# Optimization experiments

Measured on AMD Instinct MI355X. Metric: run time of the kernel, lower is better.

The kernel has to match this reference:

```python
import jax, jax.numpy as jnp
import numpy as np

B, E, R, HSZ, HEADS, PROP, RTOKS = 16, 400, 624, 512, 4, 2, 40
N = E + R            # nodes per graph = entities + relations
DFF = HSZ * HEADS    # Block FFN width (l1: hsz -> hsz*heads)


def setup_inputs() -> dict:
    key = jax.random.key(0)
    ks = jax.random.split(key, 12)
    ents = jax.random.normal(ks[0], (B, E, HSZ), jnp.float32)
    rels = jax.random.randint(ks[1], (B, R), 0, RTOKS)
    adj = jax.random.randint(ks[2], (B, N, N), 0, 2)
    # self-loops so no softmax row is fully masked
    d = jnp.arange(N)
    adj = adj.at[:, d, d].set(1)
    renc = jax.random.normal(ks[3], (RTOKS, HSZ)) * (2.0 / (RTOKS + HSZ)) ** 0.5

    def lin(k, fi, fo):  # weights stored (in, out): y = x @ W + b
        return jax.random.normal(k, (PROP, fi, fo)) * (1.0 / fi) ** 0.5

    Wq = lin(ks[4], HSZ, HSZ)
    Wk = lin(ks[5], HSZ, HSZ)
    Wv = lin(ks[6], HSZ, HSZ)
    l1_w = lin(ks[7], HSZ, DFF)
    l1_b = jnp.zeros((PROP, DFF))
    l2_w = lin(ks[8], DFF, HSZ)
    l2_b = jnp.zeros((PROP, HSZ))
    ln1_s = jnp.ones((PROP, HSZ)); ln1_b = jnp.zeros((PROP, HSZ))
    ln2_s = jnp.ones((PROP, HSZ)); ln2_b = jnp.zeros((PROP, HSZ))
    prelu_a = jnp.full((PROP, DFF), 0.25)
    return dict(ents=ents, rels=rels, adj=adj, renc=renc, Wq=Wq, Wk=Wk, Wv=Wv,
                l1_w=l1_w, l1_b=l1_b, l2_w=l2_w, l2_b=l2_b,
                ln1_s=ln1_s, ln1_b=ln1_b, ln2_s=ln2_s, ln2_b=ln2_b,
                prelu_a=prelu_a)


def _layer_norm(x, s, b, eps=1e-5):
    mu = jnp.mean(x, -1, keepdims=True)
    var = jnp.mean((x - mu) ** 2, -1, keepdims=True)
    return (x - mu) * jax.lax.rsqrt(var + eps) * s + b


def _mha(q, kv, adj, Wq, Wk, Wv):
    # GraphWriter MultiHeadAttention: split heads by contiguous chunks,
    # scale by sqrt(key_dim)=sqrt(HSZ), mask where adj==0, residual += query.
    dk = HSZ // HEADS
    Q = (q @ Wq).reshape(B, N, HEADS, dk)
    K = (kv @ Wk).reshape(B, N, HEADS, dk)
    V = (kv @ Wv).reshape(B, N, HEADS, dk)
    scores = jnp.einsum('bnhd,bmhd->bhnm', Q, K) / np.sqrt(HSZ).astype(np.float32)
    scores = jnp.where((adj == 0)[:, None, :, :], -jnp.inf, scores)
    attn = jax.nn.softmax(scores, axis=-1)
    out = jnp.einsum('bhnm,bmhd->bnhd', attn, V).reshape(B, N, HSZ)
    return out + q


def _encode(ents, rels, adj, renc, Wq, Wk, Wv, l1_w, l1_b, l2_w, l2_b,
            ln1_s, ln1_b, ln2_s, ln2_b, prelu_a):
    x = jnp.concatenate([ents, renc[rels]], axis=1)  # (B, N, HSZ)
    for j in range(PROP):  # fixed small number of propagation Blocks
        kv = jax.lax.stop_gradient(x)  # dense path wraps kv in torch.tensor(requires_grad=False)
        out = _mha(x, kv, adj, Wq[j], Wk[j], Wv[j])
        t = _layer_norm(out, ln1_s[j], ln1_b[j])
        h = t @ l1_w[j] + l1_b[j]
        h = jnp.maximum(h, 0) + prelu_a[j] * jnp.minimum(h, 0)  # PReLU
        h = h @ l2_w[j] + l2_b[j]  # dropout p=0 (eval)
        x = _layer_norm(h + t, ln2_s[j], ln2_b[j])
    return x


def reference(ents, rels, adj, renc, Wq, Wk, Wv, l1_w, l1_b, l2_w, l2_b,
              ln1_s, ln1_b, ln2_s, ln2_b, prelu_a):
    nodes = _encode(ents, rels, adj, renc, Wq, Wk, Wv, l1_w, l1_b, l2_w, l2_b,
                    ln1_s, ln1_b, ln2_s, ln2_b, prelu_a)
    glob = nodes[:, E]  # node at index ent_lens[i] (first relation node)
    node_mask = jnp.ones((B, N), dtype=bool)  # ent_lens uniform -> all valid
    return glob, nodes, node_mask
```

## Files before the change

### kernel.cpp

```cpp
#include <hip/hip_runtime.h>
#include <hip/hip_bf16.h>

typedef __bf16 bf16;
typedef __attribute__((ext_vector_type(8))) bf16 bf16x8;
typedef __attribute__((ext_vector_type(4))) float f32x4;

constexpr int B_   = 16;
constexpr int E_   = 400;
constexpr int R_   = 624;
constexpr int N_   = 1024;
constexpr int HSZ_ = 512;
constexpr int DFF_ = 2048;
constexpr int M_   = B_ * N_;

__device__ __forceinline__ void glds16(const void* g, void* l) {
    __builtin_amdgcn_global_load_lds((const __attribute__((address_space(1))) void*)g,
                                     (__attribute__((address_space(3))) void*)l,
                                     16, 0, 0);
}

__global__ __launch_bounds__(256) void transpose_all(const float* __restrict__ Wq,
                                                     const float* __restrict__ Wk,
                                                     const float* __restrict__ Wv,
                                                     const float* __restrict__ l1w,
                                                     const float* __restrict__ l2w,
                                                     bf16* __restrict__ WqkvT,
                                                     bf16* __restrict__ L1T,
                                                     bf16* __restrict__ L2T) {
    __shared__ float tile[32][33];
    int id = blockIdx.x;
    const float* in;
    bf16* out;
    int rows, cols, bx, by;
    if (id < 1536) {
        int grp = id >> 8;
        int loc = id & 255;
        bx = loc & 15; by = loc >> 4;
        rows = 512; cols = 512;
        int j = grp / 3, wsel = grp % 3;
        const float* W = (wsel == 0) ? Wq : (wsel == 1) ? Wk : Wv;
        in  = W + j * 262144;
        out = WqkvT + j * 786432 + wsel * 262144;
    } else if (id < 3584) {
        int loc = id - 1536;
        int j = loc >= 1024; loc &= 1023;
        bx = loc & 63; by = loc >> 6;
        rows = 512; cols = 2048;
        in  = l1w + j * 1048576;
        out = L1T + j * 1048576;
    } else {
        int loc = id - 3584;
        int j = loc >= 1024; loc &= 1023;
        bx = loc & 15; by = loc >> 4;
        rows = 2048; cols = 512;
        in  = l2w + j * 1048576;
        out = L2T + j * 1048576;
    }
    int tx = threadIdx.x & 31, ty = threadIdx.x >> 5;
    int c0 = bx * 32, r0 = by * 32;
    #pragma unroll
    for (int i = 0; i < 32; i += 8)
        tile[ty + i][tx] = in[(size_t)(r0 + ty + i) * cols + (c0 + tx)];
    __syncthreads();
    #pragma unroll
    for (int i = 0; i < 32; i += 8)
        out[(size_t)(c0 + ty + i) * rows + (r0 + tx)] = (bf16)tile[tx][ty + i];
}

__global__ __launch_bounds__(256) void pack_adj(const int* __restrict__ adj,
                                                unsigned* __restrict__ adjw) {
    int gid  = blockIdx.x * 4 + (threadIdx.x >> 6);
    int lane = threadIdx.x & 63;
    int w64  = gid & 15;
    int bn   = gid >> 4;
    int v = adj[(size_t)bn * N_ + w64 * 64 + lane];
    unsigned long long mask = __ballot(v != 0);
    if (lane == 0)  adjw[bn * 32 + w64 * 2]     = (unsigned)mask;
    if (lane == 32) adjw[bn * 32 + w64 * 2 + 1] = (unsigned)(mask >> 32);
}

__global__ __launch_bounds__(256) void build_x(const float* __restrict__ ents,
                                               const int* __restrict__ rels,
                                               const float* __restrict__ renc,
                                               bf16* __restrict__ x) {
    int idx  = blockIdx.x * 256 + threadIdx.x;
    int col8 = (idx & 63) * 8;
    int row  = idx >> 6;
    int b = row >> 10, n = row & 1023;
    const float* src;
    if (n < E_) src = ents + ((size_t)(b * E_ + n)) * HSZ_ + col8;
    else {
        int rt = rels[b * R_ + (n - E_)];
        src = renc + (size_t)rt * HSZ_ + col8;
    }
    float4 a = *(const float4*)src;
    float4 c = *(const float4*)(src + 4);
    bf16x8 v;
    v[0] = (bf16)a.x; v[1] = (bf16)a.y; v[2] = (bf16)a.z; v[3] = (bf16)a.w;
    v[4] = (bf16)c.x; v[5] = (bf16)c.y; v[6] = (bf16)c.z; v[7] = (bf16)c.w;
    *(bf16x8*)(x + (size_t)row * HSZ_ + col8) = v;
}

template <int MODE>
__global__ __launch_bounds__(256) void gemm_bt(const bf16* __restrict__ A,
                                               const bf16* __restrict__ Bt,
                                               const float* __restrict__ biasF,
                                               const float* __restrict__ alphaF,
                                               const bf16* __restrict__ extraB,
                                               bf16* __restrict__ outB,
                                               bf16* __restrict__ outB2,
                                               bf16* __restrict__ outB3,
                                               float* __restrict__ outF,
                                               int Nn, int Kk) {
    __shared__ bf16 As[2][128][64];
    __shared__ bf16 Bs[2][128][64];

    int nwg = gridDim.x * gridDim.y;
    int bid = blockIdx.y * gridDim.x + blockIdx.x;
    int q = nwg >> 3;
    int ng = (bid & 7) * q + (bid >> 3);
    int bx = ng % gridDim.x, by = ng / gridDim.x;

    int n0 = bx * 128, m0 = by * 128;
    int t = threadIdx.x;
    int lane = t & 63, r = lane & 15, quad = lane >> 4;
    int w = t >> 6;
    int wm = w >> 1, wn = w & 1;

    int sRow = t >> 3;
    int xr   = sRow & 7;
    int sColL = (t & 7) * 8;
    int sColG = ((t & 7) ^ xr) * 8;
    const bf16* Ag = A  + (size_t)(m0 + sRow) * Kk + sColG;
    const bf16* Bg = Bt + (size_t)(n0 + sRow) * Kk + sColG;

#define G_STAGE(p_, k0_) do {                                          \
        glds16(Ag + (k0_),           &As[p_][sRow     ][sColL]);       \
        glds16(Ag + 32 * Kk + (k0_), &As[p_][sRow + 32][sColL]);       \
        glds16(Ag + 64 * Kk + (k0_), &As[p_][sRow + 64][sColL]);       \
        glds16(Ag + 96 * Kk + (k0_), &As[p_][sRow + 96][sColL]);       \
        glds16(Bg + (k0_),           &Bs[p_][sRow     ][sColL]);       \
        glds16(Bg + 32 * Kk + (k0_), &Bs[p_][sRow + 32][sColL]);       \
        glds16(Bg + 64 * Kk + (k0_), &Bs[p_][sRow + 64][sColL]);       \
        glds16(Bg + 96 * Kk + (k0_), &Bs[p_][sRow + 96][sColL]);       \
    } while (0)

    f32x4 acc[4][4];
    #pragma unroll
    for (int mt = 0; mt < 4; mt++)
        #pragma unroll
        for (int nt = 0; nt < 4; nt++) acc[mt][nt] = (f32x4){0.f, 0.f, 0.f, 0.f};

    int xa = r & 7;

    G_STAGE(0, 0);
    int ntiles = Kk >> 6;
    for (int tt = 0; tt < ntiles; tt++) {
        int p = tt & 1;
        if (tt + 1 < ntiles) {
            G_STAGE(p ^ 1, (tt + 1) * 64);
            asm volatile("s_waitcnt vmcnt(8)" ::: "memory");
        } else {
            asm volatile("s_waitcnt vmcnt(0)" ::: "memory");
        }
        __builtin_amdgcn_s_barrier();
        __builtin_amdgcn_sched_barrier(0);
        #pragma unroll
        for (int kk = 0; kk < 64; kk += 32) {
            int pc = (((kk >> 3) + quad) ^ xa) * 8;
            bf16x8 af[4], bfr[4];
            #pragma unroll
            for (int mt = 0; mt < 4; mt++)
                af[mt] = *(const bf16x8*)&As[p][wm * 64 + mt * 16 + r][pc];
            #pragma unroll
            for (int nt = 0; nt < 4; nt++)
                bfr[nt] = *(const bf16x8*)&Bs[p][wn * 64 + nt * 16 + r][pc];
            #pragma unroll
            for (int mt = 0; mt < 4; mt++)
                #pragma unroll
                for (int nt = 0; nt < 4; nt++)
                    acc[mt][nt] = __builtin_amdgcn_mfma_f32_16x16x32_bf16(af[mt], bfr[nt], acc[mt][nt], 0, 0, 0);
        }
        __builtin_amdgcn_s_barrier();
        __builtin_amdgcn_sched_barrier(0);
    }
#undef G_STAGE

    #pragma unroll
    for (int mt = 0; mt < 4; mt++) {
        #pragma unroll
        for (int nt = 0; nt < 4; nt++) {
            #pragma unroll
            for (int i = 0; i < 4; i++) {
                int rg = m0 + wm * 64 + mt * 16 + quad * 4 + i;
                int cg = n0 + wn * 64 + nt * 16 + r;
                float v = acc[mt][nt][i];
                if (MODE == 0) {
                    outB[(size_t)rg * Nn + cg] = (bf16)v;
                } else if (MODE == 1) {
                    int bb = rg >> 10, n = rg & 1023;
                    outB[(size_t)(bb * HSZ_ + cg) * N_ + n] = (bf16)v;
                } else if (MODE == 2) {
                    v += biasF[cg];
                    float a = alphaF[cg];
                    v = v > 0.f ? v : a * v;
                    outB[(size_t)rg * Nn + cg] = (bf16)v;
                } else if (MODE == 3) {
                    v += biasF[cg] + (float)extraB[(size_t)rg * Nn + cg];
                    outF[(size_t)rg * Nn + cg] = v;
                } else {
                    if (cg < 512) {
                        outB[(size_t)rg * HSZ_ + cg] = (bf16)v;
                    } else if (cg < 1024) {
                        outB2[(size_t)rg * HSZ_ + (cg - 512)] = (bf16)v;
                    } else {
                        int bb = rg >> 10, n = rg & 1023;
                        outB3[(size_t)(bb * HSZ_ + (cg - 1024)) * N_ + n] = (bf16)v;
                    }
                }
            }
        }
    }
}

__global__ __launch_bounds__(256) void attn_fused(const bf16* __restrict__ Q,
                                                  const bf16* __restrict__ K,
                                                  const bf16* __restrict__ Vt,
                                                  const unsigned* __restrict__ adjw,
                                                  const bf16* __restrict__ xb,
                                                  float* __restrict__ tpre) {
    int blk = blockIdx.x;
    int gr = blk & 7;
    int qb = (blk >> 3) & 7;
    int gq = blk >> 6;
    int g = gq * 8 + gr;
    int b = g >> 2, h = g & 3;

    int tid = threadIdx.x;
    int w = tid >> 6, lane = tid & 63;
    int r = lane & 15, quad = lane >> 4;
    int n0 = qb * 128 + w * 32;

    __shared__ bf16 Ks[64][136];
    __shared__ bf16 Vs[128][72];
    __shared__ bf16 plds[4][32][68];

    int kRow = tid >> 4, kCol = (tid & 15) * 8;
    int vRow = tid >> 3, vCol = (tid & 7) * 8;
    const bf16* Kg = K + (size_t)(b * N_) * HSZ_ + h * 128 + (size_t)kRow * HSZ_ + kCol;
    const bf16* Vg = Vt + (size_t)(b * HSZ_ + h * 128 + vRow) * N_ + vCol;
    bf16* KsP = &Ks[kRow][kCol];
    bf16* VsP = &Vs[vRow][vCol];

    uint4 kp0, kp1, kp2, kp3, vp0, vp1, vp2, vp3;

#define ATTN_ISSUE(it_) do {                                                      \
        const bf16* kg_ = Kg + (size_t)(it_) * 64 * HSZ_;                         \
        const bf16* vg_ = Vg + (it_) * 64;                                        \
        kp0 = *(const uint4*)(kg_);                                               \
        kp1 = *(const uint4*)(kg_ + 16 * HSZ_);                                   \
        kp2 = *(const uint4*)(kg_ + 32 * HSZ_);                                   \
        kp3 = *(const uint4*)(kg_ + 48 * HSZ_);                                   \
        vp0 = *(const uint4*)(vg_);                                               \
        vp1 = *(const uint4*)(vg_ + 32 * N_);                                     \
        vp2 = *(const uint4*)(vg_ + 64 * N_);                                     \
        vp3 = *(const uint4*)(vg_ + 96 * N_);                                     \
    } while (0)

#define ATTN_COMMIT() do {                                                        \
        *(uint4*)(KsP)            = kp0;                                          \
        *(uint4*)(KsP + 16 * 136) = kp1;                                          \
        *(uint4*)(KsP + 32 * 136) = kp2;                                          \
        *(uint4*)(KsP + 48 * 136) = kp3;                                          \
        *(uint4*)(VsP)            = vp0;                                          \
        *(uint4*)(VsP + 32 * 72)  = vp1;                                          \
        *(uint4*)(VsP + 64 * 72)  = vp2;                                          \
        *(uint4*)(VsP + 96 * 72)  = vp3;                                          \
    } while (0)

    bf16x8 qf[2][4];
    #pragma unroll
    for (int mt = 0; mt < 2; mt++) {
        const bf16* qbase = Q + ((size_t)(b * N_ + n0 + mt * 16 + r)) * HSZ_ + h * 128;
        #pragma unroll
        for (int kc = 0; kc < 4; kc++) qf[mt][kc] = *(const bf16x8*)(qbase + kc * 32 + quad * 8);
    }

    f32x4 accv[2][8];
    #pragma unroll
    for (int mt = 0; mt < 2; mt++)
        #pragma unroll
        for (int dt = 0; dt < 8; dt++) accv[mt][dt] = (f32x4){0.f, 0.f, 0.f, 0.f};
    float tl[2][4] = {{0.f, 0.f, 0.f, 0.f}, {0.f, 0.f, 0.f, 0.f}};
    const float scale = 0.04419417382415922f;
    const float SHIFT = 12.0f;

    ATTN_ISSUE(0);
    for (int it = 0; it < 16; it++) {
        __syncthreads();
        ATTN_COMMIT();
        __syncthreads();
        if (it + 1 < 16) ATTN_ISSUE(it + 1);

        f32x4 cg[2][4];
        #pragma unroll
        for (int mt = 0; mt < 2; mt++)
            #pragma unroll
            for (int gk = 0; gk < 4; gk++) cg[mt][gk] = (f32x4){0.f, 0.f, 0.f, 0.f};
        __builtin_amdgcn_s_setprio(1);
        #pragma unroll
        for (int gk = 0; gk < 4; gk++)
            #pragma unroll
            for (int kc = 0; kc < 4; kc++) {
                bf16x8 kf = *(const bf16x8*)&Ks[gk * 16 + r][kc * 32 + quad * 8];
                cg[0][gk] = __builtin_amdgcn_mfma_f32_16x16x32_bf16(qf[0][kc], kf, cg[0][gk], 0, 0, 0);
                cg[1][gk] = __builtin_amdgcn_mfma_f32_16x16x32_bf16(qf[1][kc], kf, cg[1][gk], 0, 0, 0);
            }
        __builtin_amdgcn_s_setprio(0);
        #pragma unroll
        for (int mt = 0; mt < 2; mt++)
            #pragma unroll
            for (int i = 0; i < 4; i++) {
                int row_l = mt * 16 + quad * 4 + i;
                int row_g = n0 + row_l;
                const unsigned* aw = &adjw[((size_t)(b << 10) + row_g) * 32 + it * 2];
                unsigned wb0 = aw[0], wb1 = aw[1];
                float p0 = ((wb0 >> r) & 1u)        ? __expf(cg[mt][0][i] * scale - SHIFT) : 0.f;
                float p1 = ((wb0 >> (16 + r)) & 1u) ? __expf(cg[mt][1][i] * scale - SHIFT) : 0.f;
                float p2 = ((wb1 >> r) & 1u)        ? __expf(cg[mt][2][i] * scale - SHIFT) : 0.f;
                float p3 = ((wb1 >> (16 + r)) & 1u) ? __expf(cg[mt][3][i] * scale - SHIFT) : 0.f;
                tl[mt][i] += p0 + p1 + p2 + p3;
                plds[w][row_l][r]      = (bf16)p0;
                plds[w][row_l][16 + r] = (bf16)p1;
                plds[w][row_l][32 + r] = (bf16)p2;
                plds[w][row_l][48 + r] = (bf16)p3;
            }

        bf16x8 pf00 = *(const bf16x8*)&plds[w][r][quad * 8];
        bf16x8 pf01 = *(const bf16x8*)&plds[w][r][32 + quad * 8];
        bf16x8 pf10 = *(const bf16x8*)&plds[w][16 + r][quad * 8];
        bf16x8 pf11 = *(const bf16x8*)&plds[w][16 + r][32 + quad * 8];
        __builtin_amdgcn_s_setprio(1);
        #pragma unroll
        for (int dt = 0; dt < 8; dt++) {
            bf16x8 v0 = *(const bf16x8*)&Vs[dt * 16 + r][quad * 8];
            bf16x8 v1 = *(const bf16x8*)&Vs[dt * 16 + r][32 + quad * 8];
            accv[0][dt] = __builtin_amdgcn_mfma_f32_16x16x32_bf16(pf00, v0, accv[0][dt], 0, 0, 0);
            accv[0][dt] = __builtin_amdgcn_mfma_f32_16x16x32_bf16(pf01, v1, accv[0][dt], 0, 0, 0);
            accv[1][dt] = __builtin_amdgcn_mfma_f32_16x16x32_bf16(pf10, v0, accv[1][dt], 0, 0, 0);
            accv[1][dt] = __builtin_amdgcn_mfma_f32_16x16x32_bf16(pf11, v1, accv[1][dt], 0, 0, 0);
        }
        __builtin_amdgcn_s_setprio(0);
    }
#undef ATTN_ISSUE
#undef ATTN_COMMIT

    #pragma unroll
    for (int mt = 0; mt < 2; mt++)
        #pragma unroll
        for (int i = 0; i < 4; i++) {
            float l = tl[mt][i];
            #pragma unroll
            for (int d = 1; d < 16; d <<= 1) l += __shfl_xor(l, d, 64);
            float inv_l = 1.0f / fmaxf(l, 1e-30f);
            #pragma unroll
            for (int dt = 0; dt < 8; dt++) {
                int row = n0 + mt * 16 + quad * 4 + i;
                int col = h * 128 + dt * 16 + r;
                size_t idx = ((size_t)(b * N_ + row)) * HSZ_ + col;
                tpre[idx] = accv[mt][dt][i] * inv_l + (float)xb[idx];
            }
        }
}

template <int OUT>
__global__ __launch_bounds__(256) void lnorm_k(const float* __restrict__ in,
                                               const float* __restrict__ sc,
                                               const float* __restrict__ bi,
                                               bf16* __restrict__ outB,
                                               float* __restrict__ outF) {
    if (OUT == 1 && blockIdx.x >= 4096) {
        int idx = (blockIdx.x - 4096) * 1024 + threadIdx.x * 4;
        float4 one = {1.f, 1.f, 1.f, 1.f};
        *(float4*)&outF[(size_t)B_ * HSZ_ + (size_t)B_ * N_ * HSZ_ + idx] = one;
        return;
    }
    int row = blockIdx.x * 4 + (threadIdx.x >> 6);
    int lane = threadIdx.x & 63;
    const float* rp = in + (size_t)row * HSZ_;
    float4 a = *(const float4*)(rp + lane * 4);
    float4 b = *(const float4*)(rp + 256 + lane * 4);
    float sum = a.x + a.y + a.z + a.w + b.x + b.y + b.z + b.w;
    float sq  = a.x*a.x + a.y*a.y + a.z*a.z + a.w*a.w
              + b.x*b.x + b.y*b.y + b.z*b.z + b.w*b.w;
    #pragma unroll
    for (int d = 1; d < 64; d <<= 1) {
        sum += __shfl_xor(sum, d, 64);
        sq  += __shfl_xor(sq,  d, 64);
    }
    float mu = sum * (1.0f / HSZ_);
    float varv = fmaxf(sq * (1.0f / HSZ_) - mu * mu, 0.f);
    float rs = rsqrtf(varv + 1e-5f);
    int c0 = lane * 4;
    float va[4] = {a.x, a.y, a.z, a.w}, vb[4] = {b.x, b.y, b.z, b.w};
    if (OUT == 0) {
        bf16* op = outB + (size_t)row * HSZ_;
        #pragma unroll
        for (int k = 0; k < 4; k++) {
            op[c0 + k]       = (bf16)(((va[k] - mu) * rs) * sc[c0 + k] + bi[c0 + k]);
            op[c0 + 256 + k] = (bf16)(((vb[k] - mu) * rs) * sc[c0 + 256 + k] + bi[c0 + 256 + k]);
        }
    } else {
        float4 o1, o2;
        o1.x = ((va[0] - mu) * rs) * sc[c0 + 0] + bi[c0 + 0];
        o1.y = ((va[1] - mu) * rs) * sc[c0 + 1] + bi[c0 + 1];
        o1.z = ((va[2] - mu) * rs) * sc[c0 + 2] + bi[c0 + 2];
        o1.w = ((va[3] - mu) * rs) * sc[c0 + 3] + bi[c0 + 3];
        o2.x = ((vb[0] - mu) * rs) * sc[c0 + 256] + bi[c0 + 256];
        o2.y = ((vb[1] - mu) * rs) * sc[c0 + 257] + bi[c0 + 257];
        o2.z = ((vb[2] - mu) * rs) * sc[c0 + 258] + bi[c0 + 258];
        o2.w = ((vb[3] - mu) * rs) * sc[c0 + 259] + bi[c0 + 259];
        float* nodes = outF + (size_t)B_ * HSZ_;
        *(float4*)&nodes[(size_t)row * HSZ_ + c0]       = o1;
        *(float4*)&nodes[(size_t)row * HSZ_ + c0 + 256] = o2;
        int bb = row >> 10, n = row & 1023;
        if (n == E_) {
            *(float4*)&outF[(size_t)bb * HSZ_ + c0]       = o1;
            *(float4*)&outF[(size_t)bb * HSZ_ + c0 + 256] = o2;
        }
    }
}

extern "C" void kernel_launch(void* const* d_in, const int* in_sizes, int n_in,
                              void* d_out, int out_size, void* d_ws, size_t ws_size,
                              hipStream_t stream) {
    const float* ents = (const float*)d_in[0];
    const int*   rels = (const int*)d_in[1];
    const int*   adj  = (const int*)d_in[2];
    const float* renc = (const float*)d_in[3];
    const float* Wq   = (const float*)d_in[4];
    const float* Wk   = (const float*)d_in[5];
    const float* Wv   = (const float*)d_in[6];
    const float* l1w  = (const float*)d_in[7];
    const float* l1b  = (const float*)d_in[8];
    const float* l2w  = (const float*)d_in[9];
    const float* l2b  = (const float*)d_in[10];
    const float* ln1s = (const float*)d_in[11];
    const float* ln1b = (const float*)d_in[12];
    const float* ln2s = (const float*)d_in[13];
    const float* ln2b = (const float*)d_in[14];
    const float* pa   = (const float*)d_in[15];

    char* ws = (char*)d_ws;
    size_t o = 0;
    auto alloc = [&](size_t bytes) { void* p = ws + o; o += bytes; return p; };
    bf16*     WqkvT  = (bf16*)alloc(3145728);
    bf16*     L1T    = (bf16*)alloc(4194304);
    bf16*     L2T    = (bf16*)alloc(4194304);
    unsigned* adjw   = (unsigned*)alloc(2097152);
    bf16*     xb     = (bf16*)alloc(16777216);
    bf16*     Qb     = (bf16*)alloc(16777216);
    bf16*     Kb     = (bf16*)alloc(16777216);
    bf16*     Vt     = (bf16*)alloc(16777216);
    bf16*     tb     = (bf16*)alloc(16777216);
    bf16*     hb     = (bf16*)alloc(67108864);
    float*    f32buf = (float*)alloc(33554432);
    if (o > ws_size) return;

    transpose_all<<<5632, 256, 0, stream>>>(Wq, Wk, Wv, l1w, l2w, WqkvT, L1T, L2T);
    pack_adj<<<65536, 256, 0, stream>>>(adj, adjw);
    build_x<<<4096, 256, 0, stream>>>(ents, rels, renc, xb);

    for (int j = 0; j < 2; j++) {
        gemm_bt<4><<<dim3(12, 128), 256, 0, stream>>>(xb, WqkvT + j * 786432, nullptr, nullptr, nullptr,
                                                      Qb, Kb, Vt, nullptr, 1536, 512);
        attn_fused<<<512, 256, 0, stream>>>(Qb, Kb, Vt, adjw, xb, f32buf);
        lnorm_k<0><<<4096, 256, 0, stream>>>(f32buf, ln1s + j * 512, ln1b + j * 512, tb, nullptr);
        gemm_bt<2><<<dim3(16, 128), 256, 0, stream>>>(tb, L1T + j * 1048576, l1b + j * 2048, pa + j * 2048,
                                                      nullptr, hb, nullptr, nullptr, nullptr, 2048, 512);
        gemm_bt<3><<<dim3(4, 128), 256, 0, stream>>>(hb, L2T + j * 1048576, l2b + j * 512, nullptr,
                                                     tb, nullptr, nullptr, nullptr, f32buf, 512, 2048);
        if (j == 0)
            lnorm_k<0><<<4096, 256, 0, stream>>>(f32buf, ln2s, ln2b, xb, nullptr);
        else
            lnorm_k<1><<<4112, 256, 0, stream>>>(f32buf, ln2s + 512, ln2b + 512, nullptr, (float*)d_out);
    }
}
```

Before: 643.9 us.

## Enlarge GEMM tiles to 256x256 with 8 waves and phased prefetch

The bf16 GEMM goes from 128x128 tiles with 4 waves to 256x256 tiles with 8 waves. Each K-step is split into four barrier-separated phases that interleave LDS fragment reads, staggered global-to-LDS prefetch of the next tile, and MFMA bursts raised with s_setprio. The larger tile raises data reuse per load and cuts global traffic. In exchange it uses 128KB of LDS and more accumulator registers. It also launches far fewer workgroups (e.g. 128 for the L2 GEMM), which may underfill the 256 CUs.

```diff
diff --git a/kernel.cpp b/kernel.cpp
--- a/kernel.cpp
+++ b/kernel.cpp
@@ -102,18 +102,18 @@
 }
 
 template <int MODE>
-__global__ __launch_bounds__(256) void gemm_bt(const bf16* __restrict__ A,
-                                               const bf16* __restrict__ Bt,
-                                               const float* __restrict__ biasF,
-                                               const float* __restrict__ alphaF,
-                                               const bf16* __restrict__ extraB,
-                                               bf16* __restrict__ outB,
-                                               bf16* __restrict__ outB2,
-                                               bf16* __restrict__ outB3,
-                                               float* __restrict__ outF,
-                                               int Nn, int Kk) {
-    __shared__ bf16 As[2][128][64];
-    __shared__ bf16 Bs[2][128][64];
+__global__ __launch_bounds__(512, 2) void gemm_bt(const bf16* __restrict__ A,
+                                                  const bf16* __restrict__ Bt,
+                                                  const float* __restrict__ biasF,
+                                                  const float* __restrict__ alphaF,
+                                                  const bf16* __restrict__ extraB,
+                                                  bf16* __restrict__ outB,
+                                                  bf16* __restrict__ outB2,
+                                                  bf16* __restrict__ outB3,
+                                                  float* __restrict__ outF,
+                                                  int Nn, int Kk) {
+    __shared__ bf16 As[2][256][64];
+    __shared__ bf16 Bs[2][256][64];
 
     int nwg = gridDim.x * gridDim.y;
     int bid = blockIdx.y * gridDim.x + blockIdx.x;
@@ -121,11 +121,11 @@
     int ng = (bid & 7) * q + (bid >> 3);
     int bx = ng % gridDim.x, by = ng / gridDim.x;
 
-    int n0 = bx * 128, m0 = by * 128;
+    int n0 = bx * 256, m0 = by * 256;
     int t = threadIdx.x;
     int lane = t & 63, r = lane & 15, quad = lane >> 4;
-    int w = t >> 6;
-    int wm = w >> 1, wn = w & 1;
+    int wid = t >> 6;
+    int wr = wid >> 2, wc = wid & 3;
 
     int sRow = t >> 3;
     int xr   = sRow & 7;
@@ -134,73 +134,105 @@
     const bf16* Ag = A  + (size_t)(m0 + sRow) * Kk + sColG;
     const bf16* Bg = Bt + (size_t)(n0 + sRow) * Kk + sColG;
 
-#define G_STAGE(p_, k0_) do {                                          \
-        glds16(Ag + (k0_),           &As[p_][sRow     ][sColL]);       \
-        glds16(Ag + 32 * Kk + (k0_), &As[p_][sRow + 32][sColL]);       \
-        glds16(Ag + 64 * Kk + (k0_), &As[p_][sRow + 64][sColL]);       \
-        glds16(Ag + 96 * Kk + (k0_), &As[p_][sRow + 96][sColL]);       \
-        glds16(Bg + (k0_),           &Bs[p_][sRow     ][sColL]);       \
-        glds16(Bg + 32 * Kk + (k0_), &Bs[p_][sRow + 32][sColL]);       \
-        glds16(Bg + 64 * Kk + (k0_), &Bs[p_][sRow + 64][sColL]);       \
-        glds16(Bg + 96 * Kk + (k0_), &Bs[p_][sRow + 96][sColL]);       \
-    } while (0)
-
-    f32x4 acc[4][4];
-    #pragma unroll
-    for (int mt = 0; mt < 4; mt++)
+#define GL_A(p_, off_, k0_) glds16(Ag + (size_t)(off_) * Kk + (k0_), &As[p_][sRow + (off_)][sColL])
+#define GL_B(p_, off_, k0_) glds16(Bg + (size_t)(off_) * Kk + (k0_), &Bs[p_][sRow + (off_)][sColL])
+#define PHASE_BAR() do { __builtin_amdgcn_s_barrier(); __builtin_amdgcn_sched_barrier(0); } while (0)
+
+    f32x4 acc[8][4];
+    #pragma unroll
+    for (int mt = 0; mt < 8; mt++)
         #pragma unroll
         for (int nt = 0; nt < 4; nt++) acc[mt][nt] = (f32x4){0.f, 0.f, 0.f, 0.f};
 
     int xa = r & 7;
 
-    G_STAGE(0, 0);
+    GL_A(0, 0, 0); GL_A(0, 64, 0); GL_A(0, 128, 0); GL_A(0, 192, 0);
+    GL_B(0, 0, 0); GL_B(0, 64, 0); GL_B(0, 128, 0); GL_B(0, 192, 0);
+    asm volatile("s_waitcnt vmcnt(0)" ::: "memory");
+    __builtin_amdgcn_s_barrier();
+
     int ntiles = Kk >> 6;
     for (int tt = 0; tt < ntiles; tt++) {
-        int p = tt & 1;
-        if (tt + 1 < ntiles) {
-            G_STAGE(p ^ 1, (tt + 1) * 64);
-            asm volatile("s_waitcnt vmcnt(8)" ::: "memory");
-        } else {
-            asm volatile("s_waitcnt vmcnt(0)" ::: "memory");
-        }
-        __builtin_amdgcn_s_barrier();
-        __builtin_amdgcn_sched_barrier(0);
-        #pragma unroll
-        for (int kk = 0; kk < 64; kk += 32) {
-            int pc = (((kk >> 3) + quad) ^ xa) * 8;
-            bf16x8 af[4], bfr[4];
-            #pragma unroll
-            for (int mt = 0; mt < 4; mt++)
-                af[mt] = *(const bf16x8*)&As[p][wm * 64 + mt * 16 + r][pc];
+        int p = tt & 1, pn = p ^ 1;
+        bool pf = (tt + 1 < ntiles);
+        int k1 = (tt + 1) << 6;
+        bf16x8 af[4], bfr[4];
+        int pc0 = ((0 + quad) ^ xa) * 8;
+        int pc1 = ((4 + quad) ^ xa) * 8;
+
+        #pragma unroll
+        for (int i = 0; i < 4; i++) {
+            af[i]  = *(const bf16x8*)&As[p][wr * 128 + i * 16 + r][pc0];
+            bfr[i] = *(const bf16x8*)&Bs[p][wc * 64 + i * 16 + r][pc0];
+        }
+        if (pf) { GL_A(pn, 0, k1); GL_A(pn, 64, k1); GL_B(pn, 0, k1); GL_B(pn, 64, k1); }
+        PHASE_BAR();
+        __builtin_amdgcn_s_setprio(1);
+        #pragma unroll
+        for (int mt = 0; mt < 4; mt++)
             #pragma unroll
             for (int nt = 0; nt < 4; nt++)
-                bfr[nt] = *(const bf16x8*)&Bs[p][wn * 64 + nt * 16 + r][pc];
-            #pragma unroll
-            for (int mt = 0; mt < 4; mt++)
-                #pragma unroll
-                for (int nt = 0; nt < 4; nt++)
-                    acc[mt][nt] = __builtin_amdgcn_mfma_f32_16x16x32_bf16(af[mt], bfr[nt], acc[mt][nt], 0, 0, 0);
-        }
-        __builtin_amdgcn_s_barrier();
-        __builtin_amdgcn_sched_barrier(0);
-    }
-#undef G_STAGE
-
-    #pragma unroll
-    for (int mt = 0; mt < 4; mt++) {
+                acc[mt][nt] = __builtin_amdgcn_mfma_f32_16x16x32_bf16(af[mt], bfr[nt], acc[mt][nt], 0, 0, 0);
+        __builtin_amdgcn_s_setprio(0);
+        PHASE_BAR();
+
+        #pragma unroll
+        for (int i = 0; i < 4; i++)
+            af[i] = *(const bf16x8*)&As[p][wr * 128 + (i + 4) * 16 + r][pc0];
+        if (pf) { GL_A(pn, 128, k1); GL_A(pn, 192, k1); GL_B(pn, 128, k1); GL_B(pn, 192, k1); }
+        PHASE_BAR();
+        __builtin_amdgcn_s_setprio(1);
+        #pragma unroll
+        for (int mt = 0; mt < 4; mt++)
+            #pragma unroll
+            for (int nt = 0; nt < 4; nt++)
+                acc[mt + 4][nt] = __builtin_amdgcn_mfma_f32_16x16x32_bf16(af[mt], bfr[nt], acc[mt + 4][nt], 0, 0, 0);
+        __builtin_amdgcn_s_setprio(0);
+        PHASE_BAR();
+
+        #pragma unroll
+        for (int i = 0; i < 4; i++) {
+            af[i]  = *(const bf16x8*)&As[p][wr * 128 + i * 16 + r][pc1];
+            bfr[i] = *(const bf16x8*)&Bs[p][wc * 64 + i * 16 + r][pc1];
+        }
+        PHASE_BAR();
+        __builtin_amdgcn_s_setprio(1);
+        #pragma unroll
+        for (int mt = 0; mt < 4; mt++)
+            #pragma unroll
+            for (int nt = 0; nt < 4; nt++)
+                acc[mt][nt] = __builtin_amdgcn_mfma_f32_16x16x32_bf16(af[mt], bfr[nt], acc[mt][nt], 0, 0, 0);
+        __builtin_amdgcn_s_setprio(0);
+        PHASE_BAR();
+
+        #pragma unroll
+        for (int i = 0; i < 4; i++)
+            af[i] = *(const bf16x8*)&As[p][wr * 128 + (i + 4) * 16 + r][pc1];
+        PHASE_BAR();
+        __builtin_amdgcn_s_setprio(1);
+        #pragma unroll
+        for (int mt = 0; mt < 4; mt++)
+            #pragma unroll
+            for (int nt = 0; nt < 4; nt++)
+                acc[mt + 4][nt] = __builtin_amdgcn_mfma_f32_16x16x32_bf16(af[mt], bfr[nt], acc[mt + 4][nt], 0, 0, 0);
+        __builtin_amdgcn_s_setprio(0);
+        asm volatile("s_waitcnt vmcnt(0)" ::: "memory");
+        PHASE_BAR();
+    }
+#undef GL_A
+#undef GL_B
+#undef PHASE_BAR
+
+    #pragma unroll
+    for (int mt = 0; mt < 8; mt++) {
         #pragma unroll
         for (int nt = 0; nt < 4; nt++) {
             #pragma unroll
             for (int i = 0; i < 4; i++) {
-                int rg = m0 + wm * 64 + mt * 16 + quad * 4 + i;
-                int cg = n0 + wn * 64 + nt * 16 + r;
+                int rg = m0 + wr * 128 + mt * 16 + quad * 4 + i;
+                int cg = n0 + wc * 64 + nt * 16 + r;
                 float v = acc[mt][nt][i];
-                if (MODE == 0) {
-                    outB[(size_t)rg * Nn + cg] = (bf16)v;
-                } else if (MODE == 1) {
-                    int bb = rg >> 10, n = rg & 1023;
-                    outB[(size_t)(bb * HSZ_ + cg) * N_ + n] = (bf16)v;
-                } else if (MODE == 2) {
+                if (MODE == 2) {
                     v += biasF[cg];
                     float a = alphaF[cg];
                     v = v > 0.f ? v : a * v;
@@ -472,14 +504,14 @@
     build_x<<<4096, 256, 0, stream>>>(ents, rels, renc, xb);
 
     for (int j = 0; j < 2; j++) {
-        gemm_bt<4><<<dim3(12, 128), 256, 0, stream>>>(xb, WqkvT + j * 786432, nullptr, nullptr, nullptr,
-                                                      Qb, Kb, Vt, nullptr, 1536, 512);
+        gemm_bt<4><<<dim3(6, 64), 512, 0, stream>>>(xb, WqkvT + j * 786432, nullptr, nullptr, nullptr,
+                                                    Qb, Kb, Vt, nullptr, 1536, 512);
         attn_fused<<<512, 256, 0, stream>>>(Qb, Kb, Vt, adjw, xb, f32buf);
         lnorm_k<0><<<4096, 256, 0, stream>>>(f32buf, ln1s + j * 512, ln1b + j * 512, tb, nullptr);
-        gemm_bt<2><<<dim3(16, 128), 256, 0, stream>>>(tb, L1T + j * 1048576, l1b + j * 2048, pa + j * 2048,
-                                                      nullptr, hb, nullptr, nullptr, nullptr, 2048, 512);
-        gemm_bt<3><<<dim3(4, 128), 256, 0, stream>>>(hb, L2T + j * 1048576, l2b + j * 512, nullptr,
-                                                     tb, nullptr, nullptr, nullptr, f32buf, 512, 2048);
+        gemm_bt<2><<<dim3(8, 64), 512, 0, stream>>>(tb, L1T + j * 1048576, l1b + j * 2048, pa + j * 2048,
+                                                    nullptr, hb, nullptr, nullptr, nullptr, 2048, 512);
+        gemm_bt<3><<<dim3(2, 64), 512, 0, stream>>>(hb, L2T + j * 1048576, l2b + j * 512, nullptr,
+                                                    tb, nullptr, nullptr, nullptr, f32buf, 512, 2048);
         if (j == 0)
             lnorm_k<0><<<4096, 256, 0, stream>>>(f32buf, ln2s, ln2b, xb, nullptr);
         else
```

After: 705.2 us. 1.1x slower.
